# Kernel tuning notes

Hardware: AMD Instinct MI355X
Metric: run time of the kernel (lower is better)

The kernel has to match this reference:

```python
import jax, jax.numpy as jnp
import numpy as np

B, N, T, L, H = 8, 128, 256, 32, 128


def setup_inputs() -> dict:
    key = jax.random.key(0)
    k0, k1, k2, k3, k4, k5 = jax.random.split(key, 6)
    x = jax.random.uniform(k0, (B, N, T), dtype=jnp.float32)
    s = 1.0 / np.sqrt(H)  # pytorch LSTM/Linear default init scale
    W_ih = jax.random.uniform(k1, (N, 4 * H, L), minval=-s, maxval=s, dtype=jnp.float32)
    b_ih = jax.random.uniform(k2, (N, 4 * H), minval=-s, maxval=s, dtype=jnp.float32)
    b_hh = jax.random.uniform(k3, (N, 4 * H), minval=-s, maxval=s, dtype=jnp.float32)
    W_fc = jax.random.uniform(k4, (N, N, H), minval=-s, maxval=s, dtype=jnp.float32)  # [node_i, out_j, H]
    b_fc = jax.random.uniform(k5, (N, N), minval=-s, maxval=s, dtype=jnp.float32)  # [node_i, out_j]
    return {"x": x, "W_ih": W_ih, "b_ih": b_ih, "b_hh": b_hh, "W_fc": W_fc, "b_fc": b_fc}


def reference(x, W_ih, b_ih, b_hh, W_fc, b_fc):
    # x: [B, N, T]
    Bn, Nn, Tn = x.shape
    Ln = W_ih.shape[-1]
    Hh = W_fc.shape[-1]
    Ttau = Tn - Ln  # number of prediction steps (t = L .. T-1)

    # Sliding windows x[:, i, tau:tau+L] for tau = 0..Ttau-1  -> [B, N, Ttau, L]
    idx = jnp.arange(Ttau)[:, None] + jnp.arange(Ln)[None, :]  # [Ttau, L]
    xw = x[:, :, idx]

    # Single-step LSTM with zero initial state: W_hh term vanishes.
    gates = jnp.einsum('bntl,ngl->bntg', xw, W_ih) + (b_ih + b_hh)[None, :, None, :]
    gi, gf, gg, go = jnp.split(gates, 4, axis=-1)  # pytorch order: i, f, g, o
    c = jax.nn.sigmoid(gi) * jnp.tanh(gg)          # f*c0 = 0
    h = jax.nn.sigmoid(go) * jnp.tanh(c)           # [B, N, Ttau, H]

    # Per-node fc (grouped GEMM): contributions[b, tau, j, i]
    contrib = jnp.einsum('bnth,njh->btjn', h, W_fc) + b_fc.T[None, None, :, :]

    # G[b, j, i] = mean_tau contrib[b, tau, j, i] / x[b, i, L + tau]
    denom = jnp.transpose(x[:, :, Ln:], (0, 2, 1))[:, :, None, :]  # [B, Ttau, 1, N_i]
    G = jnp.mean(contrib / denom, axis=1)                          # [B, N, N]

    X_hat = jnp.sum(contrib, axis=2) + 1e-6  # [B, Ttau, N]
    return G, X_hat
```

## Files before the change

kernel.cpp:

```cpp
#include <hip/hip_runtime.h>
#include <math.h>

#define B_  8
#define N_  128
#define T_  256
#define L_  32
#define H_  128
#define TT_ 224

typedef float f2    __attribute__((ext_vector_type(2)));
typedef float f4    __attribute__((ext_vector_type(4)));
typedef float f32x4 __attribute__((ext_vector_type(4)));
typedef short bf16x8 __attribute__((ext_vector_type(8)));

#define L2E_  1.4426950408889634f
#define L2E2_ 2.8853900817779268f

__device__ __forceinline__ unsigned pk2bf(float a, float b) {
    unsigned ua = __float_as_uint(a), ub = __float_as_uint(b);
    ua = (ua + 0x7FFFu + ((ua >> 16) & 1u)) >> 16;
    ub = (ub + 0x7FFFu + ((ub >> 16) & 1u)) >> 16;
    return ua | (ub << 16);
}
__device__ __forceinline__ float aexp2(float x) {
    float r; asm("v_exp_f32 %0, %1" : "=v"(r) : "v"(x)); return r;
}
__device__ __forceinline__ float aexp2n(float x) {
    float r; asm("v_exp_f32 %0, -%1" : "=v"(r) : "v"(x)); return r;
}
__device__ __forceinline__ float arcp(float x) {
    return __builtin_amdgcn_rcpf(x);
}

__global__ __launch_bounds__(256)
void k_pre(const float* __restrict__ W_ih, const float* __restrict__ W_fc,
           const float* __restrict__ b_ih, const float* __restrict__ b_hh,
           const float* __restrict__ b_fc,
           unsigned short* __restrict__ W3sw, float* __restrict__ wsum,
           float* __restrict__ bsum, float* __restrict__ bia_g) {
    const int n   = blockIdx.x;
    const int pid = blockIdx.y;
    const int tid = threadIdx.x;
    if (pid < 6) {
        const int idx  = pid * 256 + tid;
        const int fg   = idx >> 6;
        const int lane = idx & 63;
        const int col  = lane & 15, quad = lane >> 4;
        const int g    = fg % 3, ht = fg / 3;
        const int r    = g * 128 + ht * 16 + col;
        const int sr   = r + (r >= 128 ? 128 : 0);
        const float sc = (g == 1) ? L2E2_ : L2E_;
        const f4* src = (const f4*)(W_ih + (size_t)n * 512 * L_ + sr * L_ + quad * 8);
        f4 v0 = src[0] * sc, v1 = src[1] * sc;
        uint4 out;
        out.x = pk2bf(v0.x, v0.y); out.y = pk2bf(v0.z, v0.w);
        out.z = pk2bf(v1.x, v1.y); out.w = pk2bf(v1.z, v1.w);
        *(uint4*)&W3sw[((size_t)n * 1536 + idx) * 8] = out;
    } else {
        __shared__ f4 part[8][32];
        __shared__ float bp[2];
        {
            const int h4 = tid & 31, jg = tid >> 5;
            const f4* Wf = (const f4*)(W_fc + (size_t)n * N_ * H_) + (size_t)jg * 16 * 32 + h4;
            f4 s = {0.f, 0.f, 0.f, 0.f};
            #pragma unroll
            for (int j = 0; j < 16; ++j) s += Wf[j * 32];
            part[jg][h4] = s;
        }
        if (tid < 128) {
            float bv = b_fc[n * N_ + tid];
            #pragma unroll
            for (int off = 32; off > 0; off >>= 1) bv += __shfl_down(bv, off, 64);
            if ((tid & 63) == 0) bp[tid >> 6] = bv;
        }
        for (int i = tid; i < 384; i += 256) {
            const int sr = i + (i >= 128 ? 128 : 0);
            const float sc = (i >= 128 && i < 256) ? L2E2_ : L2E_;
            bia_g[n * 384 + i] =
                (b_ih[(size_t)n * 512 + sr] + b_hh[(size_t)n * 512 + sr]) * sc;
        }
        __syncthreads();
        if (tid < 32) {
            f4 s = part[0][tid];
            #pragma unroll
            for (int jg = 1; jg < 8; ++jg) s += part[jg][tid];
            *(f4*)&wsum[n * H_ + tid * 4] = s;
        }
        if (tid == 0) bsum[n] = bp[0] + bp[1];
    }
}

__global__ __launch_bounds__(256)
__attribute__((amdgpu_waves_per_eu(4, 4)))
void k_main(const float* __restrict__ x,
            const unsigned short* __restrict__ W3sw,
            const float* __restrict__ bia_g,
            const float* __restrict__ wsum, const float* __restrict__ bsum,
            const float* __restrict__ W_fc, const float* __restrict__ b_fc,
            float* __restrict__ G, float* __restrict__ xhat) {
    const int n   = blockIdx.x;
    const int b   = blockIdx.y;
    const int tid = threadIdx.x;
    const int w    = tid >> 6;
    const int lane = tid & 63;
    const int col  = lane & 15;
    const int quad = lane >> 4;

    __shared__ float xs[258];
    __shared__ unsigned xeo[2][128];
    __shared__ float xr[TT_];
    __shared__ uint4 xA[14 * 64];
    __shared__ float xh_part[4][TT_];
    __shared__ float hd_loc[H_];
    __shared__ float red[4];

    const uint4* wsw = (const uint4*)W3sw + (size_t)n * 24 * 64 + lane;
    union { uint4 u; bf16x8 v; } bfr[2][3];
    float biaL[2][3], wshL[2];
    #pragma unroll
    for (int ht2 = 0; ht2 < 2; ++ht2) {
        const int ht = 2 * w + ht2;
        #pragma unroll
        for (int g = 0; g < 3; ++g) {
            bfr[ht2][g].u = wsw[(size_t)(ht * 3 + g) * 64];
            biaL[ht2][g]  = bia_g[n * 384 + g * 128 + ht * 16 + col];
        }
        wshL[ht2] = wsum[n * H_ + ht * 16 + col];
    }
    const float bsum_n = bsum[n];

    xs[tid] = x[((size_t)b * N_ + n) * T_ + tid];
    if (tid < 2) xs[256 + tid] = 0.f;
    __syncthreads();
    if (tid < TT_) xr[tid] = 1.0f / xs[L_ + tid];
    if (tid < 128) {
        xeo[0][tid] = pk2bf(xs[2 * tid],     xs[2 * tid + 1]);
        xeo[1][tid] = pk2bf(xs[2 * tid + 1], xs[2 * tid + 2]);
    }
    __syncthreads();
    for (int e = tid; e < 14 * 64; e += 256) {
        const int tt = e >> 6, ln = e & 63;
        const int s  = tt * 16 + (ln & 15) + (ln >> 4) * 8;
        const int p  = s & 1, base = s >> 1;
        uint4 v;
        v.x = xeo[p][base + 0]; v.y = xeo[p][base + 1];
        v.z = xeo[p][base + 2]; v.w = xeo[p][base + 3];
        xA[e] = v;
    }
    __syncthreads();

    float hd_acc[2] = {0.f, 0.f};
    const f32x4 zero4 = {0.f, 0.f, 0.f, 0.f};

    #pragma unroll 2
    for (int ttile = 0; ttile < 14; ++ttile) {
        union { uint4 u; bf16x8 v; } af;
        af.u = xA[ttile * 64 + lane];

        const f4 xr4 = *(const f4*)&xr[ttile * 16 + quad * 4];
        float px[4];

        #pragma unroll
        for (int ht2 = 0; ht2 < 2; ++ht2) {
            f32x4 ai = __builtin_amdgcn_mfma_f32_16x16x32_bf16(af.v, bfr[ht2][0].v, zero4, 0, 0, 0);
            f32x4 ag = __builtin_amdgcn_mfma_f32_16x16x32_bf16(af.v, bfr[ht2][1].v, zero4, 0, 0, 0);
            f32x4 ao = __builtin_amdgcn_mfma_f32_16x16x32_bf16(af.v, bfr[ht2][2].v, zero4, 0, 0, 0);
            #pragma unroll
            for (int pr = 0; pr < 2; ++pr) {
                f2 gi = {ai[2*pr] + biaL[ht2][0], ai[2*pr+1] + biaL[ht2][0]};
                f2 gg = {ag[2*pr] + biaL[ht2][1], ag[2*pr+1] + biaL[ht2][1]};
                f2 go = {ao[2*pr] + biaL[ht2][2], ao[2*pr+1] + biaL[ht2][2]};
                f2 e1 = {aexp2n(gi.x), aexp2n(gi.y)};
                f2 e2 = {aexp2(gg.x),  aexp2(gg.y)};
                f2 e3 = {aexp2n(go.x), aexp2n(go.y)};
                const f2 A  = (1.f + e1) * (e2 + 1.f);
                const f2 Bv = 1.f + e3;
                const f2 AB = A * Bv;
                f2 R  = {arcp(AB.x), arcp(AB.y)};
                const f2 em = e2 - 1.f;
                const f2 t  = em * R;
                const f2 c  = t * Bv;
                const f2 c2 = c * c;
                f2 Q = c2 * -0.027698f + 0.120833f;
                Q = c2 * Q - 0.331541f;
                Q = c2 * Q + 1.0f;
                const f2 hh = t * (Q * c);
                const f2 hhv = t * Q;
                hd_acc[ht2] = fmaf(hhv.x, xr4[2*pr],   hd_acc[ht2]);
                hd_acc[ht2] = fmaf(hhv.y, xr4[2*pr+1], hd_acc[ht2]);
                px[2*pr]   = hhv.x * wshL[ht2] + (ht2 ? px[2*pr]   : 0.f);
                px[2*pr+1] = hhv.y * wshL[ht2] + (ht2 ? px[2*pr+1] : 0.f);
                (void)hh;
            }
        }
        #pragma unroll
        for (int reg = 0; reg < 4; ++reg) {
            float pv = px[reg];
            pv += __shfl_xor(pv, 1, 64);
            pv += __shfl_xor(pv, 2, 64);
            pv += __shfl_xor(pv, 4, 64);
            pv += __shfl_xor(pv, 8, 64);
            if (col == 0) xh_part[w][ttile * 16 + quad * 4 + reg] = pv;
        }
    }

    #pragma unroll
    for (int ht2 = 0; ht2 < 2; ++ht2) {
        float v = hd_acc[ht2];
        v += __shfl_xor(v, 16, 64);
        v += __shfl_xor(v, 32, 64);
        if (lane < 16) hd_loc[(2 * w + ht2) * 16 + lane] = v;
    }
    {
        float dv = (tid < TT_) ? xr[tid] : 0.f;
        #pragma unroll
        for (int off = 32; off > 0; off >>= 1) dv += __shfl_down(dv, off, 64);
        if (lane == 0) red[w] = dv;
    }
    __syncthreads();

    if (tid < TT_) {
        const float v = xh_part[0][tid] + xh_part[1][tid] +
                        xh_part[2][tid] + xh_part[3][tid];
        xhat[((size_t)b * TT_ + tid) * N_ + n] = v + bsum_n + 1e-6f;
    }

    {
        const float dinv = red[0] + red[1] + red[2] + red[3];
        const int j    = tid >> 1;
        const int half = tid & 1;
        const f4* Wf = (const f4*)(W_fc + ((size_t)n * N_ + j) * H_ + half * 64);
        float s = 0.f;
        #pragma unroll
        for (int q = 0; q < 16; ++q) {
            const f4 wv = Wf[q];
            const int hb = half * 64 + q * 4;
            s = fmaf(wv.x, hd_loc[hb + 0],
                fmaf(wv.y, hd_loc[hb + 1],
                fmaf(wv.z, hd_loc[hb + 2],
                fmaf(wv.w, hd_loc[hb + 3], s))));
        }
        s += __shfl_xor(s, 1, 64);
        if (half == 0) {
            const float bj = b_fc[n * N_ + j];
            G[(size_t)b * N_ * N_ + (size_t)j * N_ + n] =
                (s + bj * dinv) * (1.0f / 224.0f);
        }
    }
}

extern "C" void kernel_launch(void* const* d_in, const int* in_sizes, int n_in,
                              void* d_out, int out_size, void* d_ws, size_t ws_size,
                              hipStream_t stream) {
    const float* x    = (const float*)d_in[0];
    const float* W_ih = (const float*)d_in[1];
    const float* b_ih = (const float*)d_in[2];
    const float* b_hh = (const float*)d_in[3];
    const float* W_fc = (const float*)d_in[4];
    const float* b_fc = (const float*)d_in[5];

    float* G    = (float*)d_out;
    float* xhat = (float*)d_out + (size_t)B_ * N_ * N_;

    unsigned short* W3sw = (unsigned short*)d_ws;
    float* wsum   = (float*)(W3sw + (size_t)N_ * 1536 * 8);
    float* bsum   = wsum + N_ * H_;
    float* bia_g  = bsum + N_;

    k_pre<<<dim3(N_, 7), dim3(256), 0, stream>>>(W_ih, W_fc, b_ih, b_hh, b_fc,
                                                 W3sw, wsum, bsum, bia_g);
    k_main<<<dim3(N_, B_), dim3(256), 0, stream>>>(x, W3sw, bia_g, wsum, bsum,
                                                   W_fc, b_fc, G, xhat);
}
```

Measured before the change: 109.5 us.

## Fold weight preprocessing kernel into main kernel to drop a launch

Removes the separate preprocessing kernel that packed W_ih to bf16, summed W_fc over outputs and combined biases. Each main-kernel block now does this for its own node directly from the fp32 inputs, keeping the W_fc column sums in shared memory. This removes one kernel launch and the workspace round trip. The cost is redundant work: the W_fc reduction (a 64KB read per node) and the W_ih conversion are repeated by all 8 batch blocks of the same node.

Result: slower. 111.9 us (+2.2%).

```diff
diff --git a/kernel.cpp b/kernel.cpp
--- a/kernel.cpp
+++ b/kernel.cpp
@@ -33,69 +33,10 @@
 }
 
 __global__ __launch_bounds__(256)
-void k_pre(const float* __restrict__ W_ih, const float* __restrict__ W_fc,
-           const float* __restrict__ b_ih, const float* __restrict__ b_hh,
-           const float* __restrict__ b_fc,
-           unsigned short* __restrict__ W3sw, float* __restrict__ wsum,
-           float* __restrict__ bsum, float* __restrict__ bia_g) {
-    const int n   = blockIdx.x;
-    const int pid = blockIdx.y;
-    const int tid = threadIdx.x;
-    if (pid < 6) {
-        const int idx  = pid * 256 + tid;
-        const int fg   = idx >> 6;
-        const int lane = idx & 63;
-        const int col  = lane & 15, quad = lane >> 4;
-        const int g    = fg % 3, ht = fg / 3;
-        const int r    = g * 128 + ht * 16 + col;
-        const int sr   = r + (r >= 128 ? 128 : 0);
-        const float sc = (g == 1) ? L2E2_ : L2E_;
-        const f4* src = (const f4*)(W_ih + (size_t)n * 512 * L_ + sr * L_ + quad * 8);
-        f4 v0 = src[0] * sc, v1 = src[1] * sc;
-        uint4 out;
-        out.x = pk2bf(v0.x, v0.y); out.y = pk2bf(v0.z, v0.w);
-        out.z = pk2bf(v1.x, v1.y); out.w = pk2bf(v1.z, v1.w);
-        *(uint4*)&W3sw[((size_t)n * 1536 + idx) * 8] = out;
-    } else {
-        __shared__ f4 part[8][32];
-        __shared__ float bp[2];
-        {
-            const int h4 = tid & 31, jg = tid >> 5;
-            const f4* Wf = (const f4*)(W_fc + (size_t)n * N_ * H_) + (size_t)jg * 16 * 32 + h4;
-            f4 s = {0.f, 0.f, 0.f, 0.f};
-            #pragma unroll
-            for (int j = 0; j < 16; ++j) s += Wf[j * 32];
-            part[jg][h4] = s;
-        }
-        if (tid < 128) {
-            float bv = b_fc[n * N_ + tid];
-            #pragma unroll
-            for (int off = 32; off > 0; off >>= 1) bv += __shfl_down(bv, off, 64);
-            if ((tid & 63) == 0) bp[tid >> 6] = bv;
-        }
-        for (int i = tid; i < 384; i += 256) {
-            const int sr = i + (i >= 128 ? 128 : 0);
-            const float sc = (i >= 128 && i < 256) ? L2E2_ : L2E_;
-            bia_g[n * 384 + i] =
-                (b_ih[(size_t)n * 512 + sr] + b_hh[(size_t)n * 512 + sr]) * sc;
-        }
-        __syncthreads();
-        if (tid < 32) {
-            f4 s = part[0][tid];
-            #pragma unroll
-            for (int jg = 1; jg < 8; ++jg) s += part[jg][tid];
-            *(f4*)&wsum[n * H_ + tid * 4] = s;
-        }
-        if (tid == 0) bsum[n] = bp[0] + bp[1];
-    }
-}
-
-__global__ __launch_bounds__(256)
 __attribute__((amdgpu_waves_per_eu(4, 4)))
 void k_main(const float* __restrict__ x,
-            const unsigned short* __restrict__ W3sw,
-            const float* __restrict__ bia_g,
-            const float* __restrict__ wsum, const float* __restrict__ bsum,
+            const float* __restrict__ W_ih,
+            const float* __restrict__ b_ih, const float* __restrict__ b_hh,
             const float* __restrict__ W_fc, const float* __restrict__ b_fc,
             float* __restrict__ G, float* __restrict__ xhat) {
     const int n   = blockIdx.x;
@@ -113,31 +54,65 @@
     __shared__ float xh_part[4][TT_];
     __shared__ float hd_loc[H_];
     __shared__ float red[4];
-
-    const uint4* wsw = (const uint4*)W3sw + (size_t)n * 24 * 64 + lane;
+    __shared__ f4 wpart[8][32];
+    __shared__ float ws_loc[H_];
+    __shared__ float bp[2];
+    __shared__ float bs_s;
+
     union { uint4 u; bf16x8 v; } bfr[2][3];
-    float biaL[2][3], wshL[2];
+    float biaL[2][3];
     #pragma unroll
     for (int ht2 = 0; ht2 < 2; ++ht2) {
         const int ht = 2 * w + ht2;
         #pragma unroll
         for (int g = 0; g < 3; ++g) {
-            bfr[ht2][g].u = wsw[(size_t)(ht * 3 + g) * 64];
-            biaL[ht2][g]  = bia_g[n * 384 + g * 128 + ht * 16 + col];
-        }
-        wshL[ht2] = wsum[n * H_ + ht * 16 + col];
-    }
-    const float bsum_n = bsum[n];
-
+            const int r  = g * 128 + ht * 16 + col;
+            const int sr = r + (r >= 128 ? 128 : 0);
+            const float sc = (g == 1) ? L2E2_ : L2E_;
+            const f4* src = (const f4*)(W_ih + (size_t)n * 512 * L_ +
+                                        (size_t)sr * L_ + quad * 8);
+            f4 v0 = src[0] * sc, v1 = src[1] * sc;
+            bfr[ht2][g].u.x = pk2bf(v0.x, v0.y);
+            bfr[ht2][g].u.y = pk2bf(v0.z, v0.w);
+            bfr[ht2][g].u.z = pk2bf(v1.x, v1.y);
+            bfr[ht2][g].u.w = pk2bf(v1.z, v1.w);
+            biaL[ht2][g] = (b_ih[(size_t)n * 512 + sr] +
+                            b_hh[(size_t)n * 512 + sr]) * sc;
+        }
+    }
+    {
+        const int h4 = tid & 31, jg = tid >> 5;
+        const f4* Wf = (const f4*)(W_fc + (size_t)n * N_ * H_) +
+                       (size_t)jg * 16 * 32 + h4;
+        f4 s = {0.f, 0.f, 0.f, 0.f};
+        #pragma unroll
+        for (int j = 0; j < 16; ++j) s += Wf[j * 32];
+        wpart[jg][h4] = s;
+    }
+    if (tid < 128) {
+        float bv = b_fc[n * N_ + tid];
+        #pragma unroll
+        for (int off = 32; off > 0; off >>= 1) bv += __shfl_down(bv, off, 64);
+        if ((tid & 63) == 0) bp[tid >> 6] = bv;
+    }
     xs[tid] = x[((size_t)b * N_ + n) * T_ + tid];
     if (tid < 2) xs[256 + tid] = 0.f;
     __syncthreads();
+
     if (tid < TT_) xr[tid] = 1.0f / xs[L_ + tid];
     if (tid < 128) {
         xeo[0][tid] = pk2bf(xs[2 * tid],     xs[2 * tid + 1]);
         xeo[1][tid] = pk2bf(xs[2 * tid + 1], xs[2 * tid + 2]);
     }
-    __syncthreads();
+    if (tid < 32) {
+        f4 s = wpart[0][tid];
+        #pragma unroll
+        for (int jg = 1; jg < 8; ++jg) s += wpart[jg][tid];
+        *(f4*)&ws_loc[tid * 4] = s;
+    }
+    if (tid == 0) bs_s = bp[0] + bp[1];
+    __syncthreads();
+
     for (int e = tid; e < 14 * 64; e += 256) {
         const int tt = e >> 6, ln = e & 63;
         const int s  = tt * 16 + (ln & 15) + (ln >> 4) * 8;
@@ -148,6 +123,11 @@
         xA[e] = v;
     }
     __syncthreads();
+
+    float wshL[2];
+    wshL[0] = ws_loc[(2 * w + 0) * 16 + col];
+    wshL[1] = ws_loc[(2 * w + 1) * 16 + col];
+    const float bsum_n = bs_s;
 
     float hd_acc[2] = {0.f, 0.f};
     const f32x4 zero4 = {0.f, 0.f, 0.f, 0.f};
@@ -184,13 +164,11 @@
                 f2 Q = c2 * -0.027698f + 0.120833f;
                 Q = c2 * Q - 0.331541f;
                 Q = c2 * Q + 1.0f;
-                const f2 hh = t * (Q * c);
                 const f2 hhv = t * Q;
                 hd_acc[ht2] = fmaf(hhv.x, xr4[2*pr],   hd_acc[ht2]);
                 hd_acc[ht2] = fmaf(hhv.y, xr4[2*pr+1], hd_acc[ht2]);
                 px[2*pr]   = hhv.x * wshL[ht2] + (ht2 ? px[2*pr]   : 0.f);
                 px[2*pr+1] = hhv.y * wshL[ht2] + (ht2 ? px[2*pr+1] : 0.f);
-                (void)hh;
             }
         }
         #pragma unroll
@@ -262,13 +240,8 @@
     float* G    = (float*)d_out;
     float* xhat = (float*)d_out + (size_t)B_ * N_ * N_;
 
-    unsigned short* W3sw = (unsigned short*)d_ws;
-    float* wsum   = (float*)(W3sw + (size_t)N_ * 1536 * 8);
-    float* bsum   = wsum + N_ * H_;
-    float* bia_g  = bsum + N_;
-
-    k_pre<<<dim3(N_, 7), dim3(256), 0, stream>>>(W_ih, W_fc, b_ih, b_hh, b_fc,
-                                                 W3sw, wsum, bsum, bia_g);
-    k_main<<<dim3(N_, B_), dim3(256), 0, stream>>>(x, W3sw, bia_g, wsum, bsum,
+    (void)d_ws; (void)ws_size;
+
+    k_main<<<dim3(N_, B_), dim3(256), 0, stream>>>(x, W_ih, b_ih, b_hh,
                                                    W_fc, b_fc, G, xhat);
 }
```
